# Performance work log

Hardware: AMD Instinct MI355X
Metric: run time of the kernel (lower is better)

Reference implementation:

```python
import jax, jax.numpy as jnp
import numpy as np

D_MODEL = 1024
NUM_HEADS = 16
ALPHA = 1.0


def setup_inputs() -> dict:
    key = jax.random.key(0)
    ks = jax.random.split(key, 6)
    bs, L, d = 2, 2048, D_MODEL
    s = 1.0 / np.sqrt(d)
    mu = jax.random.normal(ks[0], (bs, L, d), dtype=jnp.float32)
    sigma = jax.random.uniform(ks[1], (bs, L, d), dtype=jnp.float32)
    W_qkv_mu = (jax.random.normal(ks[2], (d, 3 * d), dtype=jnp.float32) * s)
    b_qkv_mu = jnp.zeros((3 * d,), dtype=jnp.float32)
    W_qkv_sigma = (jax.random.normal(ks[3], (d, 3 * d), dtype=jnp.float32) * s)
    b_qkv_sigma = jnp.zeros((3 * d,), dtype=jnp.float32)
    W_out = (jax.random.normal(ks[4], (d, d), dtype=jnp.float32) * s)
    b_out = jnp.zeros((d,), dtype=jnp.float32)
    return {"mu": mu, "sigma": sigma,
            "W_qkv_mu": W_qkv_mu, "b_qkv_mu": b_qkv_mu,
            "W_qkv_sigma": W_qkv_sigma, "b_qkv_sigma": b_qkv_sigma,
            "W_out": W_out, "b_out": b_out}


def reference(mu, sigma, W_qkv_mu, b_qkv_mu, W_qkv_sigma, b_qkv_sigma, W_out, b_out):
    bs, L, d = mu.shape
    H = NUM_HEADS
    dk = d // H

    def heads(x):  # [b, L, d] -> [b, H, L, dk]
        return x.reshape(bs, L, H, dk).transpose(0, 2, 1, 3)

    Qm, Km, Vm = (heads(t) for t in jnp.split(mu @ W_qkv_mu + b_qkv_mu, 3, axis=-1))
    Qs, Ks, Vs = (heads(t) for t in jnp.split(sigma @ W_qkv_sigma + b_qkv_sigma, 3, axis=-1))

    # Wasserstein^2 = sum((Qm-Km)^2) + sum((Qs-Ks)^2), expanded so the
    # pairwise [b,H,L,L,dk] broadcast tensor is never materialized.
    sq_q = jnp.sum(Qm * Qm, -1) + jnp.sum(Qs * Qs, -1)  # [b,H,L]
    sq_k = jnp.sum(Km * Km, -1) + jnp.sum(Ks * Ks, -1)  # [b,H,L]
    cross = (jnp.einsum('bhid,bhjd->bhij', Qm, Km)
             + jnp.einsum('bhid,bhjd->bhij', Qs, Ks))   # [b,H,L,L]
    W2 = sq_q[..., :, None] + sq_k[..., None, :] - 2.0 * cross
    W = jnp.sqrt(jnp.maximum(W2, 0.0))

    similarity = jnp.exp(-ALPHA * W)
    attn = jax.nn.softmax(similarity, axis=-1)  # softmax OVER the similarities (as in torch code)

    def merge(x):  # [b,H,L,dk] -> [b,L,d]
        return x.transpose(0, 2, 1, 3).reshape(bs, L, d)

    out_mu = merge(jnp.einsum('bhij,bhjd->bhid', attn, Vm)) @ W_out + b_out
    out_sigma = merge(jnp.einsum('bhij,bhjd->bhid', attn, Vs)) @ W_out + b_out
    return out_mu, out_sigma
```

## Files before the change

### kernel.cpp

```cpp
#include <hip/hip_runtime.h>
#include <hip/hip_bf16.h>

#define LSEQ   2048
#define DK     64
#define NH     16
#define BS     2
#define DMODEL 1024
#define BH     (BS*NH)
#define MTOT   (BS*LSEQ)

typedef __attribute__((ext_vector_type(8))) short bf16x8;
typedef __attribute__((ext_vector_type(4))) float f32x4;
typedef __attribute__((ext_vector_type(16))) float f32x16;

#define MFMA16(a,b,c) __builtin_amdgcn_mfma_f32_16x16x32_bf16((a),(b),(c),0,0,0)
#define MFMA32(a,b,c) __builtin_amdgcn_mfma_f32_32x32x16_bf16((a),(b),(c),0,0,0)
#define GLD_LDS(g,l) __builtin_amdgcn_global_load_lds((const __attribute__((address_space(1))) void*)(g), (__attribute__((address_space(3))) void*)(l), 16, 0, 0)

#define L2E   1.4426950408889634f
#define L2E2  2.0813689810056077f

__device__ __forceinline__ short f2bs(float f) {
  union { __hip_bfloat16 h; short s; } u; u.h = __float2bfloat16(f); return u.s;
}
__device__ __forceinline__ float b2f(unsigned short s) {
  union { unsigned u; float f; } v; v.u = ((unsigned)s) << 16; return v.f;
}
__device__ __forceinline__ unsigned short f2bs_c(float f) {
  union { float f; unsigned u; } v; v.f = f;
  return (unsigned short)((v.u + 0x8000u) >> 16);
}
__device__ __forceinline__ unsigned pk2c(float lo, float hi) {
  union { float f; unsigned u; } a, b; a.f = lo; b.f = hi;
  return ((a.u + 0x8000u) >> 16) | ((b.u + 0x8000u) & 0xffff0000u);
}
__device__ __forceinline__ unsigned pk2(float lo, float hi) {
  return (unsigned)(unsigned short)f2bs(lo) | (((unsigned)(unsigned short)f2bs(hi)) << 16);
}
__device__ __forceinline__ float fexp2(float x) {
  float r; asm("v_exp_f32 %0, %1" : "=v"(r) : "v"(x)); return r;
}
__device__ __forceinline__ float fexp2n(float x) {
  float r; asm("v_exp_f32 %0, -%1" : "=v"(r) : "v"(x)); return r;
}
__device__ __forceinline__ unsigned cvtpk(float lo, float hi) {
  unsigned r; asm("v_cvt_pk_bf16_f32 %0, %1, %2" : "=v"(r) : "v"(lo), "v"(hi)); return r;
}

__global__ __launch_bounds__(256) void cvt2_k(const float* __restrict__ a,
                                              const float* __restrict__ b,
                                              short* __restrict__ oa,
                                              short* __restrict__ ob, int n8) {
  int total = n8 * 2;
  for (int i = blockIdx.x * blockDim.x + threadIdx.x; i < total; i += gridDim.x * blockDim.x) {
    int sel = i >= n8;
    int j = sel ? i - n8 : i;
    const float4* p = (const float4*)(sel ? b : a) + (size_t)j * 2;
    float4 x = p[0], y = p[1];
    uint4 o;
    o.x = pk2(x.x, x.y); o.y = pk2(x.z, x.w);
    o.z = pk2(y.x, y.y); o.w = pk2(y.z, y.w);
    ((uint4*)(sel ? ob : oa))[j] = o;
  }
}

__global__ __launch_bounds__(256) void cvt_tr_all_k(
    const float* __restrict__ Wqm, const float* __restrict__ Wqs, const float* __restrict__ Wo,
    short* __restrict__ Wqm_t, short* __restrict__ Wqs_t, short* __restrict__ Wo_t) {
  __shared__ float tile[32][33];
  int id = blockIdx.x;
  const float* W; short* Wt; int Ncols, bx;
  if (id < 3072)      { W = Wqm; Wt = Wqm_t; Ncols = 3072; bx = id % 96; id /= 96; }
  else if (id < 6144) { id -= 3072; W = Wqs; Wt = Wqs_t; Ncols = 3072; bx = id % 96; id /= 96; }
  else                { id -= 6144; W = Wo;  Wt = Wo_t;  Ncols = 1024; bx = id % 32; id /= 32; }
  int n0 = bx * 32, k0 = id * 32;
  int t = threadIdx.x;
#pragma unroll
  for (int i = 0; i < 4; ++i) {
    int idx = t + i * 256; int r = idx >> 5, c = idx & 31;
    tile[r][c] = W[(size_t)(k0 + r) * Ncols + n0 + c];
  }
  __syncthreads();
#pragma unroll
  for (int i = 0; i < 4; ++i) {
    int idx = t + i * 256; int r = idx >> 5, c = idx & 31;
    Wt[(size_t)(n0 + r) * 1024 + k0 + c] = f2bs(tile[c][r]);
  }
}

__global__ __launch_bounds__(256) void qkv_gemm_k(
    const short* __restrict__ Amu, const short* __restrict__ Asg,
    const short* __restrict__ Wqm_t, const short* __restrict__ Wqs_t,
    const float* __restrict__ bqm, const float* __restrict__ bqs,
    short* __restrict__ Qm, short* __restrict__ Km, short* __restrict__ VmT,
    short* __restrict__ Qs, short* __restrict__ Ks, short* __restrict__ VsT) {
  __shared__ short As[128 * 64];
  __shared__ short Bs[128 * 64];
  int ny = blockIdx.y;
  int sg = ny >= 24;
  int n0 = (sg ? ny - 24 : ny) * 128;
  const short* A  = sg ? Asg : Amu;
  const short* Bt = sg ? Wqs_t : Wqm_t;
  const float* bias = sg ? bqs : bqm;
  short* Qb  = sg ? Qs : Qm;
  short* Kb  = sg ? Ks : Km;
  short* VTb = sg ? VsT : VmT;

  int tid = threadIdx.x, w = tid >> 6, ln = tid & 63, lg = ln >> 4, lr = ln & 15;
  int m0 = blockIdx.x * 128;
  int wr = w >> 1, wc = w & 1;
  f32x4 acc[4][4] = {};

  for (int k0 = 0; k0 < 1024; k0 += 64) {
    __syncthreads();
#pragma unroll
    for (int i = 0; i < 4; ++i) {
      int cb = w * 64 + i * 256;
      int c = cb + ln;
      GLD_LDS(A  + (size_t)(m0 + (c >> 3)) * 1024 + k0 + (c & 7) * 8, &As[cb * 8]);
      GLD_LDS(Bt + (size_t)(n0 + (c >> 3)) * 1024 + k0 + (c & 7) * 8, &Bs[cb * 8]);
    }
    __syncthreads();
#pragma unroll
    for (int kh = 0; kh < 2; ++kh) {
      bf16x8 af[4], bfr[4];
#pragma unroll
      for (int mi = 0; mi < 4; ++mi)
        af[mi] = *(const bf16x8*)&As[(wr * 64 + mi * 16 + lr) * 64 + kh * 32 + lg * 8];
#pragma unroll
      for (int ni = 0; ni < 4; ++ni)
        bfr[ni] = *(const bf16x8*)&Bs[(wc * 64 + ni * 16 + lr) * 64 + kh * 32 + lg * 8];
#pragma unroll
      for (int mi = 0; mi < 4; ++mi)
#pragma unroll
        for (int ni = 0; ni < 4; ++ni)
          acc[mi][ni] = MFMA16(af[mi], bfr[ni], acc[mi][ni]);
    }
  }

#pragma unroll
  for (int ni = 0; ni < 4; ++ni) {
    int n = n0 + wc * 64 + ni * 16 + lr;
    float bv = bias[n];
    int part = n >> 10, cc = n & 1023, hh = cc >> 6, dd = cc & 63;
#pragma unroll
    for (int mi = 0; mi < 4; ++mi) {
      int mbase = m0 + wr * 64 + mi * 16 + 4 * lg;
      float vv[4];
#pragma unroll
      for (int r = 0; r < 4; ++r) vv[r] = acc[mi][ni][r] + bv;
      if (part == 2) {
        int b = mbase >> 11, tok = mbase & 2047, bh = b * NH + hh;
        uint2 pk; pk.x = pk2c(vv[0], vv[1]); pk.y = pk2c(vv[2], vv[3]);
        *(uint2*)&VTb[((size_t)bh * DK + dd) * LSEQ + tok] = pk;
      } else {
        short* dst = (part == 0) ? Qb : Kb;
#pragma unroll
        for (int r = 0; r < 4; ++r) {
          int m = mbase + r;
          int b = m >> 11, tok = m & 2047, bh = b * NH + hh;
          dst[((size_t)bh * LSEQ + tok) * DK + dd] = (short)f2bs_c(vv[r]);
        }
      }
    }
  }
}

__global__ __launch_bounds__(256) void gemm128_k(
    const short* __restrict__ A, const short* __restrict__ Bt,
    const float* __restrict__ bias, float* __restrict__ outF) {
  __shared__ short As[128 * 64];
  __shared__ short Bs[128 * 64];
  int tid = threadIdx.x, w = tid >> 6, ln = tid & 63, lg = ln >> 4, lr = ln & 15;
  int m0 = blockIdx.x * 128, n0 = blockIdx.y * 128;
  int wr = w >> 1, wc = w & 1;
  f32x4 acc[4][4] = {};

  for (int k0 = 0; k0 < 1024; k0 += 64) {
    __syncthreads();
#pragma unroll
    for (int i = 0; i < 4; ++i) {
      int cb = w * 64 + i * 256;
      int c = cb + ln;
      GLD_LDS(A  + (size_t)(m0 + (c >> 3)) * 1024 + k0 + (c & 7) * 8, &As[cb * 8]);
      GLD_LDS(Bt + (size_t)(n0 + (c >> 3)) * 1024 + k0 + (c & 7) * 8, &Bs[cb * 8]);
    }
    __syncthreads();
#pragma unroll
    for (int kh = 0; kh < 2; ++kh) {
      bf16x8 af[4], bfr[4];
#pragma unroll
      for (int mi = 0; mi < 4; ++mi)
        af[mi] = *(const bf16x8*)&As[(wr * 64 + mi * 16 + lr) * 64 + kh * 32 + lg * 8];
#pragma unroll
      for (int ni = 0; ni < 4; ++ni)
        bfr[ni] = *(const bf16x8*)&Bs[(wc * 64 + ni * 16 + lr) * 64 + kh * 32 + lg * 8];
#pragma unroll
      for (int mi = 0; mi < 4; ++mi)
#pragma unroll
        for (int ni = 0; ni < 4; ++ni)
          acc[mi][ni] = MFMA16(af[mi], bfr[ni], acc[mi][ni]);
    }
  }

#pragma unroll
  for (int ni = 0; ni < 4; ++ni) {
    int n = n0 + wc * 64 + ni * 16 + lr;
    float bv = bias[n];
#pragma unroll
    for (int mi = 0; mi < 4; ++mi) {
      int mbase = m0 + wr * 64 + mi * 16 + 4 * lg;
#pragma unroll
      for (int r = 0; r < 4; ++r)
        outF[(size_t)(mbase + r) * 1024 + n] = acc[mi][ni][r] + bv;
    }
  }
}

__global__ __launch_bounds__(256) void norms_k(
    const short* __restrict__ Qm, const short* __restrict__ Qs,
    const short* __restrict__ Km, const short* __restrict__ Ks,
    float* __restrict__ sqq, float* __restrict__ sqk) {
  int id = blockIdx.x * 256 + threadIdx.x;
  int row = id & 65535;
  const short* p1 = (id < 65536) ? Qm : Km;
  const short* p2 = (id < 65536) ? Qs : Ks;
  float* outp = (id < 65536) ? sqq : sqk;
  const uint4* a = (const uint4*)(p1 + (size_t)row * DK);
  const uint4* b = (const uint4*)(p2 + (size_t)row * DK);
  float s = 0.f;
#pragma unroll
  for (int i = 0; i < 8; ++i) {
    uint4 x = a[i], y = b[i];
    unsigned vx[4] = {x.x, x.y, x.z, x.w};
    unsigned vy[4] = {y.x, y.y, y.z, y.w};
#pragma unroll
    for (int j = 0; j < 4; ++j) {
      float l1 = b2f((unsigned short)(vx[j] & 0xffff)), h1 = b2f((unsigned short)(vx[j] >> 16));
      float l2 = b2f((unsigned short)(vy[j] & 0xffff)), h2 = b2f((unsigned short)(vy[j] >> 16));
      s += l1 * l1 + h1 * h1 + l2 * l2 + h2 * h2;
    }
  }
  outp[row] = s * L2E2;
}

__global__ __launch_bounds__(256, 2) void attn_k(
    const short* __restrict__ Qm, const short* __restrict__ Km, const short* __restrict__ VmT,
    const short* __restrict__ Qs, const short* __restrict__ Ks, const short* __restrict__ VsT,
    const float* __restrict__ sqq, const float* __restrict__ sqk,
    short* __restrict__ Om, short* __restrict__ Os) {
  int id = blockIdx.y * 8 + blockIdx.x;
  int pid = id >> 3;
  int bh = (id & 7) * 4 + (pid >> 4);
  int q0 = (pid & 15) * 128;
  int tid = threadIdx.x, w = tid >> 6, ln = tid & 63;
  int l31 = ln & 31, h = ln >> 5;

  __shared__ __align__(16) char pool[65536];
  short* poolS = (short*)pool;

  const size_t bhQ = (size_t)bh * LSEQ * DK;

  int q = q0 + w * 32 + l31;
  bf16x8 qmf[4], qsf[4];
#pragma unroll
  for (int d = 0; d < 4; ++d) {
    qmf[d] = *(const bf16x8*)(Qm + bhQ + (size_t)q * DK + d * 16 + h * 8);
    qsf[d] = *(const bf16x8*)(Qs + bhQ + (size_t)q * DK + d * 16 + h * 8);
  }
  float sqQ = sqq[(size_t)bh * LSEQ + q];
  const float* sqkp = sqk + (size_t)bh * LSEQ;

  int rrK = tid >> 3;
  int csK = ((tid & 7) ^ (rrK & 7) ^ ((rrK >> 3) & 3)) * 8;
  const short* sKm = Km + bhQ + (size_t)rrK * DK + csK;
  const short* sKs = Ks + bhQ + (size_t)rrK * DK + csK;
  int rv = tid >> 3;
  int cv = (tid & 7) ^ (rv & 7);
  const short* sV0 = (cv < 4) ? (VmT + ((size_t)bh * DK + rv) * LSEQ + cv * 8)
                              : (VsT + ((size_t)bh * DK + rv) * LSEQ + (cv - 4) * 8);
  const short* sV1 = (cv < 4) ? (VmT + ((size_t)bh * DK + rv + 32) * LSEQ + cv * 8)
                              : (VsT + ((size_t)bh * DK + rv + 32) * LSEQ + (cv - 4) * 8);

  f32x16 acc[4] = {};
  float prs = 0.f;

  const int krow = l31;
  const int kswz = ((krow & 7) ^ ((krow >> 3) & 3)) << 4;
  const int NT = LSEQ / 32;

#define ISSUE_TILE(tt, bb) do {                                              \
    GLD_LDS(sKm + (size_t)(tt) * 2048, poolS + (bb) * 8192 + w * 512);       \
    GLD_LDS(sKs + (size_t)(tt) * 2048, poolS + (bb) * 8192 + 2048 + w * 512);\
    GLD_LDS(sV0 + (size_t)(tt) * 32,   poolS + (bb) * 8192 + 4096 + w * 512);\
    GLD_LDS(sV1 + (size_t)(tt) * 32,   poolS + (bb) * 8192 + 6144 + w * 512);\
  } while (0)

#define QK_TILE(bb, sdst) do {                                               \
    const char* kb_ = (const char*)(poolS + (bb) * 8192);                    \
    __builtin_amdgcn_s_setprio(1);                                           \
    _Pragma("unroll")                                                        \
    for (int d = 0; d < 4; ++d) {                                            \
      bf16x8 am = *(const bf16x8*)(kb_ + krow * 128 + ((d * 32 + h * 16) ^ kswz)); \
      sdst = MFMA32(am, qmf[d], sdst);                                       \
      bf16x8 as = *(const bf16x8*)(kb_ + 4096 + krow * 128 + ((d * 32 + h * 16) ^ kswz)); \
      sdst = MFMA32(as, qsf[d], sdst);                                       \
    }                                                                        \
    __builtin_amdgcn_s_setprio(0);                                           \
  } while (0)

  ISSUE_TILE(0, 0);
  ISSUE_TILE(1, 1);
  asm volatile("s_waitcnt vmcnt(4)" ::: "memory");
  asm volatile("s_barrier" ::: "memory");
  ISSUE_TILE(2, 2);

  f32x16 s_prev = {};
  QK_TILE(0, s_prev);
  f32x4 rskreg[4];
#pragma unroll
  for (int rq = 0; rq < 4; ++rq)
    rskreg[rq] = *(const f32x4*)&sqkp[8 * rq + 4 * h];

  for (int t = 1; t < NT; ++t) {
    asm volatile("s_waitcnt vmcnt(8)" ::: "memory");
    asm volatile("s_barrier" ::: "memory");
    {
      int tn = (t + 2 < NT) ? (t + 2) : (NT - 1);
      ISSUE_TILE(tn, (t + 2) & 3);
    }

    f32x16 s_cur = {};
    QK_TILE(t & 3, s_cur);

    float pv[16];
#pragma unroll
    for (int rq = 0; rq < 4; ++rq) {
#pragma unroll
      for (int r = 0; r < 4; ++r) {
        int i = rq * 4 + r;
        float w2 = fmaf(-2.f * L2E2, s_prev[i], sqQ + rskreg[rq][r]);
        float wdp = __builtin_amdgcn_sqrtf(fmaxf(w2, 0.f));
        float sim = fexp2n(wdp);
        float p = fexp2(sim * L2E);
        prs += p;
        pv[i] = p;
      }
    }
    unsigned u0 = cvtpk(pv[0], pv[1]),   u1 = cvtpk(pv[2], pv[3]);
    unsigned u2 = cvtpk(pv[4], pv[5]),   u3 = cvtpk(pv[6], pv[7]);
    unsigned u4 = cvtpk(pv[8], pv[9]),   u5 = cvtpk(pv[10], pv[11]);
    unsigned u6 = cvtpk(pv[12], pv[13]), u7 = cvtpk(pv[14], pv[15]);
    asm volatile("v_permlane32_swap_b32 %0, %1" : "+v"(u0), "+v"(u2));
    asm volatile("v_permlane32_swap_b32 %0, %1" : "+v"(u1), "+v"(u3));
    asm volatile("v_permlane32_swap_b32 %0, %1" : "+v"(u4), "+v"(u6));
    asm volatile("v_permlane32_swap_b32 %0, %1" : "+v"(u5), "+v"(u7));
    union { uint4 u; bf16x8 v; } f0, f1;
    f0.u.x = u0; f0.u.y = u1; f0.u.z = u2; f0.u.w = u3;
    f1.u.x = u4; f1.u.y = u5; f1.u.z = u6; f1.u.w = u7;

#pragma unroll
    for (int rq = 0; rq < 4; ++rq)
      rskreg[rq] = *(const f32x4*)&sqkp[t * 32 + 8 * rq + 4 * h];

    {
      const char* vb = (const char*)(poolS + ((t - 1) & 3) * 8192) + 8192;
      __builtin_amdgcn_s_setprio(1);
#pragma unroll
      for (int vblk = 0; vblk < 4; ++vblk) {
        int row = (vblk & 1) * 32 + l31;
        int cb = (vblk >> 1) * 4;
        int sw = row & 7;
        const char* rb = vb + row * 128;
        bf16x8 v0 = *(const bf16x8*)(rb + (((cb + h) ^ sw) << 4));
        bf16x8 v1 = *(const bf16x8*)(rb + (((cb + 2 + h) ^ sw) << 4));
        acc[vblk] = MFMA32(v0, f0.v, acc[vblk]);
        acc[vblk] = MFMA32(v1, f1.v, acc[vblk]);
      }
      __builtin_amdgcn_s_setprio(0);
    }

    s_prev = s_cur;
  }

  asm volatile("s_waitcnt vmcnt(0)" ::: "memory");

  {
    float pv[16];
#pragma unroll
    for (int rq = 0; rq < 4; ++rq) {
#pragma unroll
      for (int r = 0; r < 4; ++r) {
        int i = rq * 4 + r;
        float w2 = fmaf(-2.f * L2E2, s_prev[i], sqQ + rskreg[rq][r]);
        float wdp = __builtin_amdgcn_sqrtf(fmaxf(w2, 0.f));
        float sim = fexp2n(wdp);
        float p = fexp2(sim * L2E);
        prs += p;
        pv[i] = p;
      }
    }
    unsigned u0 = cvtpk(pv[0], pv[1]),   u1 = cvtpk(pv[2], pv[3]);
    unsigned u2 = cvtpk(pv[4], pv[5]),   u3 = cvtpk(pv[6], pv[7]);
    unsigned u4 = cvtpk(pv[8], pv[9]),   u5 = cvtpk(pv[10], pv[11]);
    unsigned u6 = cvtpk(pv[12], pv[13]), u7 = cvtpk(pv[14], pv[15]);
    asm volatile("v_permlane32_swap_b32 %0, %1" : "+v"(u0), "+v"(u2));
    asm volatile("v_permlane32_swap_b32 %0, %1" : "+v"(u1), "+v"(u3));
    asm volatile("v_permlane32_swap_b32 %0, %1" : "+v"(u4), "+v"(u6));
    asm volatile("v_permlane32_swap_b32 %0, %1" : "+v"(u5), "+v"(u7));
    union { uint4 u; bf16x8 v; } f0, f1;
    f0.u.x = u0; f0.u.y = u1; f0.u.z = u2; f0.u.w = u3;
    f1.u.x = u4; f1.u.y = u5; f1.u.z = u6; f1.u.w = u7;

    const char* vb = (const char*)(poolS + ((NT - 1) & 3) * 8192) + 8192;
#pragma unroll
    for (int vblk = 0; vblk < 4; ++vblk) {
      int row = (vblk & 1) * 32 + l31;
      int cb = (vblk >> 1) * 4;
      int sw = row & 7;
      const char* rb = vb + row * 128;
      bf16x8 v0 = *(const bf16x8*)(rb + (((cb + h) ^ sw) << 4));
      bf16x8 v1 = *(const bf16x8*)(rb + (((cb + 2 + h) ^ sw) << 4));
      acc[vblk] = MFMA32(v0, f0.v, acc[vblk]);
      acc[vblk] = MFMA32(v1, f1.v, acc[vblk]);
    }
  }

  prs += __shfl_xor(prs, 32);
  float inv = 1.f / prs;

  int b = bh >> 4, hh = bh & 15;
  size_t orow = ((size_t)(b * LSEQ + q)) * DMODEL + hh * DK;
#pragma unroll
  for (int vblk = 0; vblk < 4; ++vblk) {
    short* obuf = (vblk < 2) ? Om : Os;
    int vbase = (vblk & 1) * 32 + 4 * h;
#pragma unroll
    for (int rq = 0; rq < 4; ++rq) {
      float o0 = acc[vblk][rq * 4 + 0] * inv;
      float o1 = acc[vblk][rq * 4 + 1] * inv;
      float o2 = acc[vblk][rq * 4 + 2] * inv;
      float o3 = acc[vblk][rq * 4 + 3] * inv;
      uint2 pk; pk.x = pk2c(o0, o1); pk.y = pk2c(o2, o3);
      *(uint2*)(obuf + orow + vbase + 8 * rq) = pk;
    }
  }
#undef ISSUE_TILE
#undef QK_TILE
}

extern "C" void kernel_launch(void* const* d_in, const int* in_sizes, int n_in,
                              void* d_out, int out_size, void* d_ws, size_t ws_size,
                              hipStream_t stream) {
  const float* mu    = (const float*)d_in[0];
  const float* sigma = (const float*)d_in[1];
  const float* Wqm   = (const float*)d_in[2];
  const float* bqm   = (const float*)d_in[3];
  const float* Wqs   = (const float*)d_in[4];
  const float* bqs   = (const float*)d_in[5];
  const float* Wo    = (const float*)d_in[6];
  const float* bo    = (const float*)d_in[7];
  float* out = (float*)d_out;
  char* ws = (char*)d_ws;
  const size_t MB = 1u << 20;

  short* Amu   = (short*)(ws + 0);
  short* Asg   = (short*)(ws + 8 * MB);
  short* Wqm_t = (short*)(ws + 16 * MB);
  short* Wqs_t = (short*)(ws + 22 * MB);
  short* Wo_t  = (short*)(ws + 28 * MB);
  short* Qm    = (short*)(ws + 30 * MB);
  short* Km    = (short*)(ws + 38 * MB);
  short* VmT   = (short*)(ws + 46 * MB);
  short* Qs    = (short*)(ws + 54 * MB);
  short* Ks    = (short*)(ws + 62 * MB);
  short* VsT   = (short*)(ws + 70 * MB);
  float* sqq   = (float*)(ws + 78 * MB);
  float* sqk   = (float*)(ws + 78 * MB + 256 * 1024);
  short* Om = Amu;
  short* Os = Asg;

  cvt2_k<<<2048, 256, 0, stream>>>(mu, sigma, Amu, Asg, MTOT * DMODEL / 8);
  cvt_tr_all_k<<<7168, 256, 0, stream>>>(Wqm, Wqs, Wo, Wqm_t, Wqs_t, Wo_t);

  qkv_gemm_k<<<dim3(32, 48), 256, 0, stream>>>(Amu, Asg, Wqm_t, Wqs_t, bqm, bqs,
                                               Qm, Km, VmT, Qs, Ks, VsT);

  norms_k<<<512, 256, 0, stream>>>(Qm, Qs, Km, Ks, sqq, sqk);

  attn_k<<<dim3(8, 64), 256, 0, stream>>>(Qm, Km, VmT, Qs, Ks, VsT, sqq, sqk, Om, Os);

  gemm128_k<<<dim3(64, 8), 256, 0, stream>>>(Om, Wo_t, bo, out);
}
```

Before: 229.4 us.

## Merge conversion kernels and split QK MFMA chains to overlap with softmax

Folds the activation bf16 conversion kernel into the weight transpose-convert kernel, so one launch does both. In the attention loop, the mu and sigma QK products now go into separate accumulators. The sigma half is issued after the exp/sqrt work of the previous tile, so MFMA runs alongside VALU transcendental work. The sqQ term is also pre-added into the key-norm registers. The cost is one more f32x16 accumulator live across the loop, which raises register pressure, plus an extra add per element.

```diff
diff --git a/kernel.cpp b/kernel.cpp
--- a/kernel.cpp
+++ b/kernel.cpp
@@ -47,34 +47,34 @@
   unsigned r; asm("v_cvt_pk_bf16_f32 %0, %1, %2" : "=v"(r) : "v"(lo), "v"(hi)); return r;
 }
 
-__global__ __launch_bounds__(256) void cvt2_k(const float* __restrict__ a,
-                                              const float* __restrict__ b,
-                                              short* __restrict__ oa,
-                                              short* __restrict__ ob, int n8) {
-  int total = n8 * 2;
-  for (int i = blockIdx.x * blockDim.x + threadIdx.x; i < total; i += gridDim.x * blockDim.x) {
-    int sel = i >= n8;
-    int j = sel ? i - n8 : i;
-    const float4* p = (const float4*)(sel ? b : a) + (size_t)j * 2;
-    float4 x = p[0], y = p[1];
-    uint4 o;
-    o.x = pk2(x.x, x.y); o.y = pk2(x.z, x.w);
-    o.z = pk2(y.x, y.y); o.w = pk2(y.z, y.w);
-    ((uint4*)(sel ? ob : oa))[j] = o;
-  }
-}
-
-__global__ __launch_bounds__(256) void cvt_tr_all_k(
+__global__ __launch_bounds__(256) void cvt_all_k(
+    const float* __restrict__ mu, const float* __restrict__ sigma,
+    short* __restrict__ Amu, short* __restrict__ Asg,
     const float* __restrict__ Wqm, const float* __restrict__ Wqs, const float* __restrict__ Wo,
     short* __restrict__ Wqm_t, short* __restrict__ Wqs_t, short* __restrict__ Wo_t) {
+  int id = blockIdx.x;
+  int t = threadIdx.x;
+  if (id >= 7168) {
+    int n8 = MTOT * DMODEL / 8;
+    int total = n8 * 2;
+    for (int i = (id - 7168) * 256 + t; i < total; i += 2048 * 256) {
+      int sel = i >= n8;
+      int j = sel ? i - n8 : i;
+      const float4* p = (const float4*)(sel ? sigma : mu) + (size_t)j * 2;
+      float4 x = p[0], y = p[1];
+      uint4 o;
+      o.x = pk2(x.x, x.y); o.y = pk2(x.z, x.w);
+      o.z = pk2(y.x, y.y); o.w = pk2(y.z, y.w);
+      ((uint4*)(sel ? Asg : Amu))[j] = o;
+    }
+    return;
+  }
   __shared__ float tile[32][33];
-  int id = blockIdx.x;
   const float* W; short* Wt; int Ncols, bx;
   if (id < 3072)      { W = Wqm; Wt = Wqm_t; Ncols = 3072; bx = id % 96; id /= 96; }
   else if (id < 6144) { id -= 3072; W = Wqs; Wt = Wqs_t; Ncols = 3072; bx = id % 96; id /= 96; }
   else                { id -= 6144; W = Wo;  Wt = Wo_t;  Ncols = 1024; bx = id % 32; id /= 32; }
   int n0 = bx * 32, k0 = id * 32;
-  int t = threadIdx.x;
 #pragma unroll
   for (int i = 0; i < 4; ++i) {
     int idx = t + i * 256; int r = idx >> 5, c = idx & 31;
@@ -296,13 +296,21 @@
     GLD_LDS(sV1 + (size_t)(tt) * 32,   poolS + (bb) * 8192 + 6144 + w * 512);\
   } while (0)
 
-#define QK_TILE(bb, sdst) do {                                               \
+#define QK_M(bb, sdst) do {                                                  \
     const char* kb_ = (const char*)(poolS + (bb) * 8192);                    \
     __builtin_amdgcn_s_setprio(1);                                           \
     _Pragma("unroll")                                                        \
     for (int d = 0; d < 4; ++d) {                                            \
       bf16x8 am = *(const bf16x8*)(kb_ + krow * 128 + ((d * 32 + h * 16) ^ kswz)); \
       sdst = MFMA32(am, qmf[d], sdst);                                       \
+    }                                                                        \
+    __builtin_amdgcn_s_setprio(0);                                           \
+  } while (0)
+#define QK_S(bb, sdst) do {                                                  \
+    const char* kb_ = (const char*)(poolS + (bb) * 8192);                    \
+    __builtin_amdgcn_s_setprio(1);                                           \
+    _Pragma("unroll")                                                        \
+    for (int d = 0; d < 4; ++d) {                                            \
       bf16x8 as = *(const bf16x8*)(kb_ + 4096 + krow * 128 + ((d * 32 + h * 16) ^ kswz)); \
       sdst = MFMA32(as, qsf[d], sdst);                                       \
     }                                                                        \
@@ -315,12 +323,16 @@
   asm volatile("s_barrier" ::: "memory");
   ISSUE_TILE(2, 2);
 
-  f32x16 s_prev = {};
-  QK_TILE(0, s_prev);
+  f32x16 sm_prev = {}, ss_prev = {};
+  QK_M(0, sm_prev);
+  QK_S(0, ss_prev);
   f32x4 rskreg[4];
 #pragma unroll
-  for (int rq = 0; rq < 4; ++rq)
+  for (int rq = 0; rq < 4; ++rq) {
     rskreg[rq] = *(const f32x4*)&sqkp[8 * rq + 4 * h];
+#pragma unroll
+    for (int r = 0; r < 4; ++r) rskreg[rq][r] += sqQ;
+  }
 
   for (int t = 1; t < NT; ++t) {
     asm volatile("s_waitcnt vmcnt(8)" ::: "memory");
@@ -330,8 +342,8 @@
       ISSUE_TILE(tn, (t + 2) & 3);
     }
 
-    f32x16 s_cur = {};
-    QK_TILE(t & 3, s_cur);
+    f32x16 sm_cur = {}, ss_cur = {};
+    QK_M(t & 3, sm_cur);
 
     float pv[16];
 #pragma unroll
@@ -339,7 +351,7 @@
 #pragma unroll
       for (int r = 0; r < 4; ++r) {
         int i = rq * 4 + r;
-        float w2 = fmaf(-2.f * L2E2, s_prev[i], sqQ + rskreg[rq][r]);
+        float w2 = fmaf(-2.f * L2E2, sm_prev[i] + ss_prev[i], rskreg[rq][r]);
         float wdp = __builtin_amdgcn_sqrtf(fmaxf(w2, 0.f));
         float sim = fexp2n(wdp);
         float p = fexp2(sim * L2E);
@@ -347,6 +359,9 @@
         pv[i] = p;
       }
     }
+
+    QK_S(t & 3, ss_cur);
+
     unsigned u0 = cvtpk(pv[0], pv[1]),   u1 = cvtpk(pv[2], pv[3]);
     unsigned u2 = cvtpk(pv[4], pv[5]),   u3 = cvtpk(pv[6], pv[7]);
     unsigned u4 = cvtpk(pv[8], pv[9]),   u5 = cvtpk(pv[10], pv[11]);
@@ -360,8 +375,11 @@
     f1.u.x = u4; f1.u.y = u5; f1.u.z = u6; f1.u.w = u7;
 
 #pragma unroll
-    for (int rq = 0; rq < 4; ++rq)
+    for (int rq = 0; rq < 4; ++rq) {
       rskreg[rq] = *(const f32x4*)&sqkp[t * 32 + 8 * rq + 4 * h];
+#pragma unroll
+      for (int r = 0; r < 4; ++r) rskreg[rq][r] += sqQ;
+    }
 
     {
       const char* vb = (const char*)(poolS + ((t - 1) & 3) * 8192) + 8192;
@@ -380,7 +398,8 @@
       __builtin_amdgcn_s_setprio(0);
     }
 
-    s_prev = s_cur;
+    sm_prev = sm_cur;
+    ss_prev = ss_cur;
   }
 
   asm volatile("s_waitcnt vmcnt(0)" ::: "memory");
@@ -392,7 +411,7 @@
 #pragma unroll
       for (int r = 0; r < 4; ++r) {
         int i = rq * 4 + r;
-        float w2 = fmaf(-2.f * L2E2, s_prev[i], sqQ + rskreg[rq][r]);
+        float w2 = fmaf(-2.f * L2E2, sm_prev[i] + ss_prev[i], rskreg[rq][r]);
         float wdp = __builtin_amdgcn_sqrtf(fmaxf(w2, 0.f));
         float sim = fexp2n(wdp);
         float p = fexp2(sim * L2E);
@@ -446,7 +465,8 @@
     }
   }
 #undef ISSUE_TILE
-#undef QK_TILE
+#undef QK_M
+#undef QK_S
 }
 
 extern "C" void kernel_launch(void* const* d_in, const int* in_sizes, int n_in,
@@ -480,8 +500,8 @@
   short* Om = Amu;
   short* Os = Asg;
 
-  cvt2_k<<<2048, 256, 0, stream>>>(mu, sigma, Amu, Asg, MTOT * DMODEL / 8);
-  cvt_tr_all_k<<<7168, 256, 0, stream>>>(Wqm, Wqs, Wo, Wqm_t, Wqs_t, Wo_t);
+  cvt_all_k<<<9216, 256, 0, stream>>>(mu, sigma, Amu, Asg,
+                                      Wqm, Wqs, Wo, Wqm_t, Wqs_t, Wo_t);
 
   qkv_gemm_k<<<dim3(32, 48), 256, 0, stream>>>(Amu, Asg, Wqm_t, Wqs_t, bqm, bqs,
                                                Qm, Km, VmT, Qs, Ks, VsT);
```

Measured after the change: 231.0 us. Within noise of the previous version (+0.7%).
